# Performance work log

Hardware: AMD Instinct MI355X
Metric: run time of the kernel (lower is better)

## Reference

```python
import jax, jax.numpy as jnp
import numpy as np

N = 50000       # nodes
E = 600000      # directed edges (before self loops)
IN_CH = 128
HID = 64
HEADS = 2
H2_CH = HID // HEADS  # 32
OUT_CH = 96
NEG_SLOPE = 0.2


def _w(key, shape):
    fan_in = shape[-1]
    return jax.random.normal(key, shape, dtype=jnp.float32) / np.sqrt(fan_in).astype(np.float32)


def setup_inputs() -> dict:
    key = jax.random.key(0)
    ks = jax.random.split(key, 20)
    x = jax.random.normal(ks[0], (N, IN_CH), dtype=jnp.float32)
    edge_index = jax.random.randint(ks[1], (2, E), 0, N, dtype=jnp.int32)
    batch = jnp.zeros((N,), dtype=jnp.int32)
    return {
        "x": x, "edge_index": edge_index, "batch": batch,
        # lin_in 128->128
        "Win": _w(ks[2], (IN_CH, IN_CH)), "b_in": jnp.zeros((IN_CH,), jnp.float32),
        # conv1: GATv2Conv(128 -> 64, heads=2, concat=True)
        "Wl1": _w(ks[3], (HEADS * HID, IN_CH)), "bl1": jnp.zeros((HEADS * HID,), jnp.float32),
        "Wr1": _w(ks[4], (HEADS * HID, IN_CH)), "br1": jnp.zeros((HEADS * HID,), jnp.float32),
        "att1": _w(ks[5], (HEADS, HID)), "bias1": jnp.zeros((HEADS * HID,), jnp.float32),
        # conv2: GATv2Conv(128 -> 32, heads=1, concat=True)
        "Wl2": _w(ks[6], (H2_CH, HEADS * HID)), "bl2": jnp.zeros((H2_CH,), jnp.float32),
        "Wr2": _w(ks[7], (H2_CH, HEADS * HID)), "br2": jnp.zeros((H2_CH,), jnp.float32),
        "att2": _w(ks[8], (1, H2_CH)), "bias2": jnp.zeros((H2_CH,), jnp.float32),
        # final linear 32 -> 96
        "Wout": _w(ks[9], (OUT_CH, H2_CH)), "b_out": jnp.zeros((OUT_CH,), jnp.float32),
    }


def _segment_softmax(logits, seg, num):
    # logits: [E, H] grouped by seg (destination node); every node has a self loop.
    m = jax.ops.segment_max(logits, seg, num_segments=num)
    ex = jnp.exp(logits - m[seg])
    s = jax.ops.segment_sum(ex, seg, num_segments=num)
    return ex / s[seg]


def _gatv2_conv(h, Wl, bl, Wr, br, att, bias, src, dst, heads, ch):
    n = h.shape[0]
    xl = (h @ Wl.T + bl).reshape(n, heads, ch)  # source-side (x_j)
    xr = (h @ Wr.T + br).reshape(n, heads, ch)  # target-side (x_i)
    e = jax.nn.leaky_relu(xl[src] + xr[dst], NEG_SLOPE)       # [E, H, C]
    logits = jnp.einsum('ehc,hc->eh', e, att)                  # [E, H]
    alpha = _segment_softmax(logits, dst, n)                   # softmax over in-edges per dst
    out = jax.ops.segment_sum(alpha[:, :, None] * xl[src], dst, num_segments=n)
    return out.reshape(n, heads * ch) + bias


def reference(x, edge_index, batch, Win, b_in, Wl1, bl1, Wr1, br1, att1, bias1,
              Wl2, bl2, Wr2, br2, att2, bias2, Wout, b_out):
    n = x.shape[0]
    loops = jnp.arange(n, dtype=edge_index.dtype)
    src = jnp.concatenate([edge_index[0], loops])  # add_self_loops=True (PyG default)
    dst = jnp.concatenate([edge_index[1], loops])
    h = x @ Win.T + b_in
    h = jax.nn.relu(_gatv2_conv(h, Wl1, bl1, Wr1, br1, att1, bias1, src, dst, HEADS, HID))
    h = jax.nn.relu(_gatv2_conv(h, Wl2, bl2, Wr2, br2, att2, bias2, src, dst, 1, H2_CH))
    num_graphs = 1
    sums = jax.ops.segment_sum(h, batch, num_segments=num_graphs)          # [G, 32]
    cnt = jax.ops.segment_sum(jnp.ones((n,), h.dtype), batch, num_segments=num_graphs)
    pooled = sums / cnt[:, None]
    return pooled @ Wout.T + b_out  # [G, 96]
```

## Files before the change

### kernel.cpp

```cpp
#include <hip/hip_runtime.h>
#include <hip/hip_bf16.h>
#include <math.h>


#define NEG_SLOPE 0.2f
#define LOG2E 1.4426950408889634f
#define NREP 16
#define ELLW 64
#define CH 2048
#define CAPB 8192

typedef __attribute__((ext_vector_type(8))) short bf16x8;
typedef __attribute__((ext_vector_type(4))) float f32x4;

__device__ __forceinline__ float leaky(float t) { return fmaxf(t, NEG_SLOPE * t); }
__device__ __forceinline__ float bf2f(unsigned short u) {
    return __uint_as_float((unsigned)u << 16);
}
__device__ __forceinline__ short f2bf(float f) {
    __hip_bfloat16 h = __float2bfloat16(f);
    return *reinterpret_cast<short*>(&h);
}
__device__ __forceinline__ short f2bf_fast(float f) {
    return (short)((__float_as_uint(f) + 0x8000u) >> 16);
}

template <int CTRL>
__device__ __forceinline__ float dppadd(float v) {
    int t = __builtin_amdgcn_update_dpp(0, __float_as_int(v), CTRL, 0xF, 0xF, true);
    return v + __int_as_float(t);
}

__global__ __launch_bounds__(256) void prep_kernel(const float* __restrict__ Win,
                                                   const float* __restrict__ b_in,
                                                   const float* __restrict__ Wl1,
                                                   const float* __restrict__ bl1,
                                                   const float* __restrict__ Wr1,
                                                   const float* __restrict__ br1,
                                                   const float* __restrict__ Wl2,
                                                   const float* __restrict__ bl2,
                                                   const float* __restrict__ Wr2,
                                                   const float* __restrict__ br2,
                                                   unsigned short* __restrict__ Wcat1,
                                                   float* __restrict__ bcat1,
                                                   unsigned short* __restrict__ Wcat2,
                                                   float* __restrict__ bcat2,
                                                   int* __restrict__ bucketCnt,
                                                   float* __restrict__ pooledR, int N) {
    int b = blockIdx.x, t = threadIdx.x;
    if (b < 128) {
        int half = t >> 7;
        int k = t & 127;
        int o = b * 2 + half;
        const float* Wx = (o < 128) ? Wl1 : Wr1;
        const float* bx = (o < 128) ? bl1 : br1;
        int oo = o & 127;
        float acc = 0.f;
#pragma unroll 16
        for (int j = 0; j < 128; ++j)
            acc = fmaf(Wx[oo * 128 + j], Win[j * 128 + k], acc);
        Wcat1[o * 128 + k] = (unsigned short)f2bf(acc);

        __shared__ float red[256];
        red[t] = Wx[oo * 128 + k] * b_in[k];
        __syncthreads();
        for (int off = 64; off > 0; off >>= 1) {
            if (k < off) red[t] += red[t + off];
            __syncthreads();
        }
        if (k == 0) bcat1[o] = red[half * 128] + bx[oo];
    } else if (b < 160) {
        int i = (b - 128) * 256 + t;
        int m = i >> 7, kk = i & 127;
        float v = (m < 32) ? Wl2[m * 128 + kk] : Wr2[(m - 32) * 128 + kk];
        Wcat2[i] = (unsigned short)f2bf(v);
        if (b == 128 && t < 64) bcat2[t] = (t < 32) ? bl2[t] : br2[t - 32];
    } else if (b == 160) {
        if (t < 256) bucketCnt[t] = 0;
    } else {
        int i = (b - 161) * 256 + t;
        if (i < NREP * 32) pooledR[i] = 0.f;
    }
}

__global__ __launch_bounds__(256) void part_kernel(const int* __restrict__ ei,
                                                   int* __restrict__ bucketCnt,
                                                   unsigned int* __restrict__ region,
                                                   int E) {
    __shared__ int hist[256];
    __shared__ int base[256];
    __shared__ int off[256];
    int b = blockIdx.x, t = threadIdx.x;
    int e0 = b * CH;
    int e1 = e0 + CH; if (e1 > E) e1 = E;

    hist[t] = 0;
    __syncthreads();
    for (int e = e0 + t; e < e1; e += 256) {
        int d = ei[E + e];
        atomicAdd(&hist[d >> 8], 1);
    }
    __syncthreads();
    int h = hist[t];
    base[t] = (h > 0) ? atomicAdd(&bucketCnt[t], h) : 0;
    off[t] = 0;
    __syncthreads();
    for (int e = e0 + t; e < e1; e += 256) {
        int s = ei[e];
        int d = ei[E + e];
        int bk = d >> 8;
        int p = base[bk] + atomicAdd(&off[bk], 1);
        if (p < CAPB)
            region[(size_t)bk * CAPB + p] = (unsigned)s | ((unsigned)(d & 255) << 16);
    }
}

__global__ __launch_bounds__(256) void ellb_kernel(const unsigned int* __restrict__ region,
                                                   const int* __restrict__ bucketCnt,
                                                   unsigned short* __restrict__ ell,
                                                   int* __restrict__ deg, int N) {
    __shared__ unsigned short tile[256 * ELLW];
    __shared__ int cur[256];
    int nb = blockIdx.x, t = threadIdx.x;
    cur[t] = 0;
    __syncthreads();
    int cnt = bucketCnt[nb];
    if (cnt > CAPB) cnt = CAPB;
    for (int i = t; i < cnt; i += 256) {
        unsigned p = region[(size_t)nb * CAPB + i];
        int doff = p >> 16;
        int s = p & 0xFFFF;
        int r = atomicAdd(&cur[doff], 1);
        if (r < ELLW) tile[doff * ELLW + r] = (unsigned short)s;
    }
    __syncthreads();
    int node = nb * 256 + t;
    int dgl = cur[t];
    if (dgl > ELLW) dgl = ELLW;
    if (node < N) {
        deg[node] = dgl;
        int pe = dgl + 8; if (pe > ELLW) pe = ELLW;
        for (int r = dgl; r < pe; ++r) tile[t * ELLW + r] = (unsigned short)node;
    }
    __syncthreads();
    const uint4* tl = (const uint4*)tile;
    uint4* gl = (uint4*)(ell + (size_t)nb * 256 * ELLW);
#pragma unroll
    for (int k = 0; k < 8; ++k) {
        int idx = t + k * 256;
        int row = idx >> 3;
        if (nb * 256 + row < N) gl[idx] = tl[idx];
    }
}

__global__ __launch_bounds__(256) void gemm1_kernel(const float* __restrict__ x,
                                                    const unsigned short* __restrict__ W,
                                                    const float* __restrict__ bias,
                                                    unsigned short* __restrict__ XL,
                                                    unsigned short* __restrict__ XR, int N) {
    const int w = threadIdx.x >> 6;
    const int lane = threadIdx.x & 63;
    const int ln = lane & 15;
    const int quad = lane >> 4;
    const int nb = blockIdx.x * 32;
    const int c0 = w * 64;

    int rows[2];
#pragma unroll
    for (int rt = 0; rt < 2; ++rt) {
        int n = nb + rt * 16 + ln;
        rows[rt] = n < N ? n : N - 1;
    }

    float4 araw[2][4][2];
#pragma unroll
    for (int rt = 0; rt < 2; ++rt)
#pragma unroll
        for (int kc = 0; kc < 4; ++kc) {
            const float* p = x + (size_t)rows[rt] * 128 + kc * 32 + quad * 8;
            araw[rt][kc][0] = *(const float4*)p;
            araw[rt][kc][1] = *(const float4*)(p + 4);
        }
    bf16x8 a[2][4];
#pragma unroll
    for (int rt = 0; rt < 2; ++rt)
#pragma unroll
        for (int kc = 0; kc < 4; ++kc) {
            float4 u = araw[rt][kc][0], v = araw[rt][kc][1];
            a[rt][kc][0] = f2bf_fast(u.x); a[rt][kc][1] = f2bf_fast(u.y);
            a[rt][kc][2] = f2bf_fast(u.z); a[rt][kc][3] = f2bf_fast(u.w);
            a[rt][kc][4] = f2bf_fast(v.x); a[rt][kc][5] = f2bf_fast(v.y);
            a[rt][kc][6] = f2bf_fast(v.z); a[rt][kc][7] = f2bf_fast(v.w);
        }

    f32x4 acc[2][4];
#pragma unroll
    for (int rt = 0; rt < 2; ++rt)
#pragma unroll
        for (int ct = 0; ct < 4; ++ct) acc[rt][ct] = (f32x4){0.f, 0.f, 0.f, 0.f};

#pragma unroll
    for (int kc = 0; kc < 4; ++kc) {
        const int k0 = kc * 32 + quad * 8;
        bf16x8 wv[4];
#pragma unroll
        for (int ct = 0; ct < 4; ++ct)
            wv[ct] = *(const bf16x8*)(W + (size_t)(c0 + ct * 16 + ln) * 128 + k0);
#pragma unroll
        for (int rt = 0; rt < 2; ++rt)
#pragma unroll
            for (int ct = 0; ct < 4; ++ct)
                acc[rt][ct] = __builtin_amdgcn_mfma_f32_16x16x32_bf16(wv[ct], a[rt][kc], acc[rt][ct], 0, 0, 0);
    }

#pragma unroll
    for (int rt = 0; rt < 2; ++rt) {
        int n = nb + rt * 16 + ln;
        if (n >= N) continue;
#pragma unroll
        for (int ct = 0; ct < 4; ++ct) {
            int cb = c0 + ct * 16 + quad * 4;
            float4 bv = *(const float4*)&bias[cb];
            ushort4 o;
            o.x = (unsigned short)f2bf(acc[rt][ct][0] + bv.x);
            o.y = (unsigned short)f2bf(acc[rt][ct][1] + bv.y);
            o.z = (unsigned short)f2bf(acc[rt][ct][2] + bv.z);
            o.w = (unsigned short)f2bf(acc[rt][ct][3] + bv.w);
            if (cb < 128) *(ushort4*)&XL[(size_t)n * 128 + cb] = o;
            else          *(ushort4*)&XR[(size_t)n * 128 + cb - 128] = o;
        }
    }
}

__global__ __launch_bounds__(256) void node_conv1(const unsigned short* __restrict__ XL,
                                                  const unsigned short* __restrict__ XR,
                                                  const int* __restrict__ deg,
                                                  const unsigned short* __restrict__ ell,
                                                  const float* __restrict__ att,
                                                  const float* __restrict__ bias,
                                                  const unsigned short* __restrict__ Wcat2,
                                                  const float* __restrict__ bcat2,
                                                  unsigned short* __restrict__ XL2,
                                                  unsigned short* __restrict__ XR2, int N) {
    __shared__ unsigned short hsh[8 * 128];
    int g = threadIdx.x >> 5;
    int d = blockIdx.x * 8 + g;
    int l = threadIdx.x & 31;
    int c0 = 4 * l;

    if (d < N) {
        const unsigned short* row = ell + (size_t)d * ELLW;
        int re = deg[d];

        float4 attv = *(const float4*)&att[c0];
        attv.x *= LOG2E; attv.y *= LOG2E; attv.z *= LOG2E; attv.w *= LOG2E;
        ushort4 xru = *(const ushort4*)&XR[(size_t)d * 128 + c0];
        float xr0 = bf2f(xru.x), xr1 = bf2f(xru.y), xr2 = bf2f(xru.z), xr3 = bf2f(xru.w);

        float ssum, a0, a1, a2, a3;
        float w_self, xs0, xs1, xs2, xs3;

#define LOADX1(s) (*(const ushort4*)&XL[(size_t)(s) * 128 + c0])
#define PROC1(xu)                                                          \
    {                                                                      \
        float x0 = bf2f(xu.x), x1 = bf2f(xu.y), x2 = bf2f(xu.z), x3 = bf2f(xu.w); \
        float p = leaky(x0 + xr0) * attv.x;                                \
        p = fmaf(leaky(x1 + xr1), attv.y, p);                              \
        p = fmaf(leaky(x2 + xr2), attv.z, p);                              \
        p = fmaf(leaky(x3 + xr3), attv.w, p);                              \
        p = dppadd<0xB1>(p);                                               \
        p = dppadd<0x4E>(p);                                               \
        p = dppadd<0x124>(p);                                              \
        p = dppadd<0x128>(p);                                              \
        float wgt = exp2f(p);                                              \
        ssum += wgt;                                                       \
        a0 = fmaf(wgt, x0, a0); a1 = fmaf(wgt, x1, a1);                    \
        a2 = fmaf(wgt, x2, a2); a3 = fmaf(wgt, x3, a3);                    \
    }

        {
            ushort4 xu = *(const ushort4*)&XL[(size_t)d * 128 + c0];
            xs0 = bf2f(xu.x); xs1 = bf2f(xu.y); xs2 = bf2f(xu.z); xs3 = bf2f(xu.w);
            float p = leaky(xs0 + xr0) * attv.x;
            p = fmaf(leaky(xs1 + xr1), attv.y, p);
            p = fmaf(leaky(xs2 + xr2), attv.z, p);
            p = fmaf(leaky(xs3 + xr3), attv.w, p);
            p = dppadd<0xB1>(p);
            p = dppadd<0x4E>(p);
            p = dppadd<0x124>(p);
            p = dppadd<0x128>(p);
            w_self = exp2f(p);
            ssum = w_self;
            a0 = w_self * xs0; a1 = w_self * xs1;
            a2 = w_self * xs2; a3 = w_self * xs3;
        }
        if (re > 0) {
            int rp = (re + 3) & ~3;
            ushort4 i0 = *(const ushort4*)&row[0];
            ushort4 b0 = LOADX1(i0.x), b1 = LOADX1(i0.y), b2 = LOADX1(i0.z), b3 = LOADX1(i0.w);
            for (int j = 0; j < rp; j += 4) {
                int j4 = j + 4 < ELLW - 3 ? j + 4 : ELLW - 4;
                ushort4 i1 = *(const ushort4*)&row[j4];
                ushort4 n0 = LOADX1(i1.x), n1 = LOADX1(i1.y), n2 = LOADX1(i1.z), n3 = LOADX1(i1.w);
                PROC1(b0);
                PROC1(b1);
                PROC1(b2);
                PROC1(b3);
                b0 = n0; b1 = n1; b2 = n2; b3 = n3;
            }
            float kw = (float)(rp - re) * w_self;
            ssum -= kw;
            a0 = fmaf(-kw, xs0, a0); a1 = fmaf(-kw, xs1, a1);
            a2 = fmaf(-kw, xs2, a2); a3 = fmaf(-kw, xs3, a3);
        }
#undef PROC1
#undef LOADX1

        float inv = 1.0f / ssum;
        float4 bv = *(const float4*)&bias[c0];
        float r0 = fmaf(a0, inv, bv.x), r1 = fmaf(a1, inv, bv.y);
        float r2 = fmaf(a2, inv, bv.z), r3 = fmaf(a3, inv, bv.w);
        ushort4 o;
        o.x = (unsigned short)f2bf(r0 > 0.f ? r0 : 0.f);
        o.y = (unsigned short)f2bf(r1 > 0.f ? r1 : 0.f);
        o.z = (unsigned short)f2bf(r2 > 0.f ? r2 : 0.f);
        o.w = (unsigned short)f2bf(r3 > 0.f ? r3 : 0.f);
        *(ushort4*)&hsh[g * 128 + c0] = o;
    } else {
        *(ushort4*)&hsh[g * 128 + c0] = make_ushort4(0, 0, 0, 0);
    }
    __syncthreads();

    {
        int w = threadIdx.x >> 6;
        int lane = threadIdx.x & 63;
        int ln = lane & 15;
        int quad = lane >> 4;
        f32x4 acc = (f32x4){0.f, 0.f, 0.f, 0.f};
#pragma unroll
        for (int kc = 0; kc < 4; ++kc) {
            int k0 = kc * 32 + quad * 8;
            bf16x8 a;
            if (ln < 8) a = *(const bf16x8*)&hsh[ln * 128 + k0];
            else        a = (bf16x8){0, 0, 0, 0, 0, 0, 0, 0};
            bf16x8 wv = *(const bf16x8*)(Wcat2 + (size_t)(w * 16 + ln) * 128 + k0);
            acc = __builtin_amdgcn_mfma_f32_16x16x32_bf16(wv, a, acc, 0, 0, 0);
        }
        int n = blockIdx.x * 8 + ln;
        if (ln < 8 && n < N) {
            int cb = w * 16 + quad * 4;
            float4 bv = *(const float4*)&bcat2[cb];
            ushort4 o;
            o.x = (unsigned short)f2bf(acc[0] + bv.x);
            o.y = (unsigned short)f2bf(acc[1] + bv.y);
            o.z = (unsigned short)f2bf(acc[2] + bv.z);
            o.w = (unsigned short)f2bf(acc[3] + bv.w);
            if (cb < 32) *(ushort4*)&XL2[(size_t)n * 32 + cb] = o;
            else         *(ushort4*)&XR2[(size_t)n * 32 + cb - 32] = o;
        }
    }
}

__global__ __launch_bounds__(256) void node_conv2(const unsigned short* __restrict__ XL,
                                                  const unsigned short* __restrict__ XR,
                                                  const int* __restrict__ deg,
                                                  const unsigned short* __restrict__ ell,
                                                  const float* __restrict__ att,
                                                  const float* __restrict__ bias,
                                                  float* __restrict__ pooledR, int N) {
    __shared__ float psh[32];
    if (threadIdx.x < 32) psh[threadIdx.x] = 0.0f;
    __syncthreads();

    int slot = threadIdx.x >> 3;
    int l = threadIdx.x & 7;
    int c0 = 4 * l;
    float4 attv = *(const float4*)&att[c0];
    attv.x *= LOG2E; attv.y *= LOG2E; attv.z *= LOG2E; attv.w *= LOG2E;
    float4 bv = *(const float4*)&bias[c0];
    float p0 = 0.f, p1 = 0.f, p2 = 0.f, p3 = 0.f;

#define LOADX2(s) (*(const ushort4*)&XL[(size_t)(s) * 32 + c0])
#define PROC2(xu)                                                          \
    {                                                                      \
        float x0 = bf2f(xu.x), x1 = bf2f(xu.y), x2 = bf2f(xu.z), x3 = bf2f(xu.w); \
        float p = leaky(x0 + xr0) * attv.x;                                \
        p = fmaf(leaky(x1 + xr1), attv.y, p);                              \
        p = fmaf(leaky(x2 + xr2), attv.z, p);                              \
        p = fmaf(leaky(x3 + xr3), attv.w, p);                              \
        p = dppadd<0xB1>(p);                                               \
        p = dppadd<0x4E>(p);                                               \
        p = dppadd<0x141>(p);                                              \
        float wgt = exp2f(p);                                              \
        ssum += wgt;                                                       \
        a0 = fmaf(wgt, x0, a0); a1 = fmaf(wgt, x1, a1);                    \
        a2 = fmaf(wgt, x2, a2); a3 = fmaf(wgt, x3, a3);                    \
    }

    for (int d = blockIdx.x * 32 + slot; d < N; d += gridDim.x * 32) {
        const unsigned short* row = ell + (size_t)d * ELLW;
        int re = deg[d];
        ushort4 xru = *(const ushort4*)&XR[(size_t)d * 32 + c0];
        float xr0 = bf2f(xru.x), xr1 = bf2f(xru.y), xr2 = bf2f(xru.z), xr3 = bf2f(xru.w);
        float ssum, a0, a1, a2, a3;
        float w_self, xs0, xs1, xs2, xs3;

        {
            ushort4 xu = *(const ushort4*)&XL[(size_t)d * 32 + c0];
            xs0 = bf2f(xu.x); xs1 = bf2f(xu.y); xs2 = bf2f(xu.z); xs3 = bf2f(xu.w);
            float p = leaky(xs0 + xr0) * attv.x;
            p = fmaf(leaky(xs1 + xr1), attv.y, p);
            p = fmaf(leaky(xs2 + xr2), attv.z, p);
            p = fmaf(leaky(xs3 + xr3), attv.w, p);
            p = dppadd<0xB1>(p);
            p = dppadd<0x4E>(p);
            p = dppadd<0x141>(p);
            w_self = exp2f(p);
            ssum = w_self;
            a0 = w_self * xs0; a1 = w_self * xs1;
            a2 = w_self * xs2; a3 = w_self * xs3;
        }
        if (re > 0) {
            int rp = (re + 3) & ~3;
            ushort4 i0 = *(const ushort4*)&row[0];
            ushort4 b0 = LOADX2(i0.x), b1 = LOADX2(i0.y), b2 = LOADX2(i0.z), b3 = LOADX2(i0.w);
            for (int j = 0; j < rp; j += 4) {
                int j4 = j + 4 < ELLW - 3 ? j + 4 : ELLW - 4;
                ushort4 i1 = *(const ushort4*)&row[j4];
                ushort4 n0 = LOADX2(i1.x), n1 = LOADX2(i1.y), n2 = LOADX2(i1.z), n3 = LOADX2(i1.w);
                PROC2(b0);
                PROC2(b1);
                PROC2(b2);
                PROC2(b3);
                b0 = n0; b1 = n1; b2 = n2; b3 = n3;
            }
            float kw = (float)(rp - re) * w_self;
            ssum -= kw;
            a0 = fmaf(-kw, xs0, a0); a1 = fmaf(-kw, xs1, a1);
            a2 = fmaf(-kw, xs2, a2); a3 = fmaf(-kw, xs3, a3);
        }

        float inv = 1.0f / ssum;
        float r0 = fmaf(a0, inv, bv.x), r1 = fmaf(a1, inv, bv.y);
        float r2 = fmaf(a2, inv, bv.z), r3 = fmaf(a3, inv, bv.w);
        p0 += r0 > 0.f ? r0 : 0.f;
        p1 += r1 > 0.f ? r1 : 0.f;
        p2 += r2 > 0.f ? r2 : 0.f;
        p3 += r3 > 0.f ? r3 : 0.f;
    }
#undef PROC2
#undef LOADX2
    atomicAdd(&psh[c0 + 0], p0);
    atomicAdd(&psh[c0 + 1], p1);
    atomicAdd(&psh[c0 + 2], p2);
    atomicAdd(&psh[c0 + 3], p3);
    __syncthreads();
    float* rep = pooledR + (blockIdx.x & (NREP - 1)) * 32;
    if (threadIdx.x < 32) atomicAdd(&rep[threadIdx.x], psh[threadIdx.x]);
}

__global__ void out_kernel(const float* __restrict__ pooledR, const float* __restrict__ Wout,
                           const float* __restrict__ b_out, float* __restrict__ out, int N) {
    __shared__ float psum[32];
    if (threadIdx.x < 32) {
        float tot = 0.f;
#pragma unroll
        for (int r = 0; r < NREP; ++r) tot += pooledR[r * 32 + threadIdx.x];
        psum[threadIdx.x] = tot;
    }
    __syncthreads();
    int m = threadIdx.x;
    if (m < 96) {
        float invN = 1.0f / (float)N;
        float s = b_out[m];
#pragma unroll
        for (int c = 0; c < 32; ++c) s += (psum[c] * invN) * Wout[m * 32 + c];
        out[m] = s;
    }
}

extern "C" void kernel_launch(void* const* d_in, const int* in_sizes, int n_in,
                              void* d_out, int out_size, void* d_ws, size_t ws_size,
                              hipStream_t stream) {
    const float* x     = (const float*)d_in[0];
    const int*   ei    = (const int*)d_in[1];
    const float* Win   = (const float*)d_in[3];
    const float* b_in  = (const float*)d_in[4];
    const float* Wl1   = (const float*)d_in[5];
    const float* bl1   = (const float*)d_in[6];
    const float* Wr1   = (const float*)d_in[7];
    const float* br1   = (const float*)d_in[8];
    const float* att1  = (const float*)d_in[9];
    const float* bias1 = (const float*)d_in[10];
    const float* Wl2   = (const float*)d_in[11];
    const float* bl2   = (const float*)d_in[12];
    const float* Wr2   = (const float*)d_in[13];
    const float* br2   = (const float*)d_in[14];
    const float* att2  = (const float*)d_in[15];
    const float* bias2 = (const float*)d_in[16];
    const float* Wout  = (const float*)d_in[17];
    const float* b_out = (const float*)d_in[18];
    float* out = (float*)d_out;

    int N = in_sizes[0] / 128;
    int E = in_sizes[1] / 2;
    int NB = (N + 255) >> 8;

    char* wsb = (char*)d_ws;
    size_t off = 0;
    auto alloc = [&](size_t bytes) { void* p = wsb + off; off += (bytes + 255) & ~(size_t)255; return p; };

    unsigned short* XL1   = (unsigned short*)alloc((size_t)N * 128 * 2);
    unsigned short* XR1   = (unsigned short*)alloc((size_t)N * 128 * 2);
    unsigned short* XL2   = (unsigned short*)alloc((size_t)N * 32 * 2);
    unsigned short* XR2   = (unsigned short*)alloc((size_t)N * 32 * 2);
    unsigned short* Wcat1 = (unsigned short*)alloc(256 * 128 * 2);
    unsigned short* Wcat2 = (unsigned short*)alloc(64 * 128 * 2);
    float* bcat1   = (float*)alloc(256 * 4);
    float* bcat2   = (float*)alloc(64 * 4);
    float* pooledR = (float*)alloc(NREP * 32 * 4);
    int* bucketCnt = (int*)alloc(256 * 4);
    int* deg       = (int*)alloc((size_t)N * 4);
    unsigned int* region = (unsigned int*)alloc((size_t)NB * CAPB * 4);
    unsigned short* ell  = (unsigned short*)alloc((size_t)N * ELLW * 2);

    prep_kernel<<<163, 256, 0, stream>>>(Win, b_in, Wl1, bl1, Wr1, br1,
                                         Wl2, bl2, Wr2, br2,
                                         Wcat1, bcat1, Wcat2, bcat2, bucketCnt, pooledR, N);
    part_kernel<<<(E + CH - 1) / CH, 256, 0, stream>>>(ei, bucketCnt, region, E);
    ellb_kernel<<<NB, 256, 0, stream>>>(region, bucketCnt, ell, deg, N);
    gemm1_kernel<<<(N + 31) / 32, 256, 0, stream>>>(x, Wcat1, bcat1, XL1, XR1, N);
    node_conv1<<<(N + 7) / 8, 256, 0, stream>>>(XL1, XR1, deg, ell, att1, bias1,
                                                Wcat2, bcat2, XL2, XR2, N);
    node_conv2<<<1024, 256, 0, stream>>>(XL2, XR2, deg, ell, att2, bias2, pooledR, N);
    out_kernel<<<1, 128, 0, stream>>>(pooledR, Wout, b_out, out, N);
}
```

Measured before the change: 213.1 us.

## Fuse gemm1 blocks into partition and ELL-build kernels for overlap

The input projection GEMM is split in half, and each half runs as extra blocks inside the edge-partition and ELL-build kernels. This removes one launch and lets the latency-bound graph-preprocessing blocks overlap with the compute-heavy GEMM blocks. The node_conv2 grid also grows from 1024 blocks to one block per 32 nodes. A side effect is that the GEMM blocks in the second fused kernel reserve the ELL tile's large shared-memory allocation, which may lower their occupancy.

```diff
diff --git a/kernel.cpp b/kernel.cpp
--- a/kernel.cpp
+++ b/kernel.cpp
@@ -83,86 +83,16 @@
     }
 }
 
-__global__ __launch_bounds__(256) void part_kernel(const int* __restrict__ ei,
-                                                   int* __restrict__ bucketCnt,
-                                                   unsigned int* __restrict__ region,
-                                                   int E) {
-    __shared__ int hist[256];
-    __shared__ int base[256];
-    __shared__ int off[256];
-    int b = blockIdx.x, t = threadIdx.x;
-    int e0 = b * CH;
-    int e1 = e0 + CH; if (e1 > E) e1 = E;
-
-    hist[t] = 0;
-    __syncthreads();
-    for (int e = e0 + t; e < e1; e += 256) {
-        int d = ei[E + e];
-        atomicAdd(&hist[d >> 8], 1);
-    }
-    __syncthreads();
-    int h = hist[t];
-    base[t] = (h > 0) ? atomicAdd(&bucketCnt[t], h) : 0;
-    off[t] = 0;
-    __syncthreads();
-    for (int e = e0 + t; e < e1; e += 256) {
-        int s = ei[e];
-        int d = ei[E + e];
-        int bk = d >> 8;
-        int p = base[bk] + atomicAdd(&off[bk], 1);
-        if (p < CAPB)
-            region[(size_t)bk * CAPB + p] = (unsigned)s | ((unsigned)(d & 255) << 16);
-    }
-}
-
-__global__ __launch_bounds__(256) void ellb_kernel(const unsigned int* __restrict__ region,
-                                                   const int* __restrict__ bucketCnt,
-                                                   unsigned short* __restrict__ ell,
-                                                   int* __restrict__ deg, int N) {
-    __shared__ unsigned short tile[256 * ELLW];
-    __shared__ int cur[256];
-    int nb = blockIdx.x, t = threadIdx.x;
-    cur[t] = 0;
-    __syncthreads();
-    int cnt = bucketCnt[nb];
-    if (cnt > CAPB) cnt = CAPB;
-    for (int i = t; i < cnt; i += 256) {
-        unsigned p = region[(size_t)nb * CAPB + i];
-        int doff = p >> 16;
-        int s = p & 0xFFFF;
-        int r = atomicAdd(&cur[doff], 1);
-        if (r < ELLW) tile[doff * ELLW + r] = (unsigned short)s;
-    }
-    __syncthreads();
-    int node = nb * 256 + t;
-    int dgl = cur[t];
-    if (dgl > ELLW) dgl = ELLW;
-    if (node < N) {
-        deg[node] = dgl;
-        int pe = dgl + 8; if (pe > ELLW) pe = ELLW;
-        for (int r = dgl; r < pe; ++r) tile[t * ELLW + r] = (unsigned short)node;
-    }
-    __syncthreads();
-    const uint4* tl = (const uint4*)tile;
-    uint4* gl = (uint4*)(ell + (size_t)nb * 256 * ELLW);
-#pragma unroll
-    for (int k = 0; k < 8; ++k) {
-        int idx = t + k * 256;
-        int row = idx >> 3;
-        if (nb * 256 + row < N) gl[idx] = tl[idx];
-    }
-}
-
-__global__ __launch_bounds__(256) void gemm1_kernel(const float* __restrict__ x,
-                                                    const unsigned short* __restrict__ W,
-                                                    const float* __restrict__ bias,
-                                                    unsigned short* __restrict__ XL,
-                                                    unsigned short* __restrict__ XR, int N) {
+__device__ __forceinline__ void gemm1_body(const float* __restrict__ x,
+                                           const unsigned short* __restrict__ W,
+                                           const float* __restrict__ bias,
+                                           unsigned short* __restrict__ XL,
+                                           unsigned short* __restrict__ XR,
+                                           int N, int nb) {
     const int w = threadIdx.x >> 6;
     const int lane = threadIdx.x & 63;
     const int ln = lane & 15;
     const int quad = lane >> 4;
-    const int nb = blockIdx.x * 32;
     const int c0 = w * 64;
 
     int rows[2];
@@ -229,6 +159,96 @@
             if (cb < 128) *(ushort4*)&XL[(size_t)n * 128 + cb] = o;
             else          *(ushort4*)&XR[(size_t)n * 128 + cb - 128] = o;
         }
+    }
+}
+
+__global__ __launch_bounds__(256) void fuse1_kernel(const int* __restrict__ ei,
+                                                    int* __restrict__ bucketCnt,
+                                                    unsigned int* __restrict__ region,
+                                                    int E,
+                                                    const float* __restrict__ x,
+                                                    const unsigned short* __restrict__ W,
+                                                    const float* __restrict__ bias,
+                                                    unsigned short* __restrict__ XL,
+                                                    unsigned short* __restrict__ XR,
+                                                    int N, int PB) {
+    __shared__ int hist[256];
+    __shared__ int base[256];
+    __shared__ int off[256];
+    if (blockIdx.x >= PB) {
+        gemm1_body(x, W, bias, XL, XR, N, (blockIdx.x - PB) * 32);
+        return;
+    }
+    int b = blockIdx.x, t = threadIdx.x;
+    int e0 = b * CH;
+    int e1 = e0 + CH; if (e1 > E) e1 = E;
+
+    hist[t] = 0;
+    __syncthreads();
+    for (int e = e0 + t; e < e1; e += 256) {
+        int d = ei[E + e];
+        atomicAdd(&hist[d >> 8], 1);
+    }
+    __syncthreads();
+    int h = hist[t];
+    base[t] = (h > 0) ? atomicAdd(&bucketCnt[t], h) : 0;
+    off[t] = 0;
+    __syncthreads();
+    for (int e = e0 + t; e < e1; e += 256) {
+        int s = ei[e];
+        int d = ei[E + e];
+        int bk = d >> 8;
+        int p = base[bk] + atomicAdd(&off[bk], 1);
+        if (p < CAPB)
+            region[(size_t)bk * CAPB + p] = (unsigned)s | ((unsigned)(d & 255) << 16);
+    }
+}
+
+__global__ __launch_bounds__(256) void fuse2_kernel(const unsigned int* __restrict__ region,
+                                                    const int* __restrict__ bucketCnt,
+                                                    unsigned short* __restrict__ ell,
+                                                    int* __restrict__ deg,
+                                                    const float* __restrict__ x,
+                                                    const unsigned short* __restrict__ W,
+                                                    const float* __restrict__ bias,
+                                                    unsigned short* __restrict__ XL,
+                                                    unsigned short* __restrict__ XR,
+                                                    int N, int NB, int nodeOff) {
+    __shared__ unsigned short tile[256 * ELLW];
+    __shared__ int cur[256];
+    if (blockIdx.x >= NB) {
+        gemm1_body(x, W, bias, XL, XR, N, nodeOff + (blockIdx.x - NB) * 32);
+        return;
+    }
+    int nb = blockIdx.x, t = threadIdx.x;
+    cur[t] = 0;
+    __syncthreads();
+    int cnt = bucketCnt[nb];
+    if (cnt > CAPB) cnt = CAPB;
+    for (int i = t; i < cnt; i += 256) {
+        unsigned p = region[(size_t)nb * CAPB + i];
+        int doff = p >> 16;
+        int s = p & 0xFFFF;
+        int r = atomicAdd(&cur[doff], 1);
+        if (r < ELLW) tile[doff * ELLW + r] = (unsigned short)s;
+    }
+    __syncthreads();
+    int node = nb * 256 + t;
+    int dgl = cur[t];
+    if (dgl > ELLW) dgl = ELLW;
+    if (node < N) {
+        deg[node] = dgl;
+        int pe = dgl + 8; if (pe > ELLW) pe = ELLW;
+        for (int r = dgl; r < pe; ++r) tile[t * ELLW + r] = (unsigned short)node;
+    }
+    __syncthreads();
+    const uint4* tl = (const uint4*)tile;
+    uint4* gl = (uint4*)(ell + (size_t)nb * 256 * ELLW);
+#pragma unroll
+    for (int k = 0; k < 8; ++k) {
+        int idx = t + k * 256;
+        int row = idx >> 3;
+        if (nb * 256 + row < N) gl[idx] = tl[idx];
     }
 }
 
@@ -524,14 +544,20 @@
     unsigned int* region = (unsigned int*)alloc((size_t)NB * CAPB * 4);
     unsigned short* ell  = (unsigned short*)alloc((size_t)N * ELLW * 2);
 
+    int PB  = (E + CH - 1) / CH;
+    int GT  = (N + 31) / 32;
+    int GB1 = GT / 2;
+    int GB2 = GT - GB1;
+
     prep_kernel<<<163, 256, 0, stream>>>(Win, b_in, Wl1, bl1, Wr1, br1,
                                          Wl2, bl2, Wr2, br2,
                                          Wcat1, bcat1, Wcat2, bcat2, bucketCnt, pooledR, N);
-    part_kernel<<<(E + CH - 1) / CH, 256, 0, stream>>>(ei, bucketCnt, region, E);
-    ellb_kernel<<<NB, 256, 0, stream>>>(region, bucketCnt, ell, deg, N);
-    gemm1_kernel<<<(N + 31) / 32, 256, 0, stream>>>(x, Wcat1, bcat1, XL1, XR1, N);
+    fuse1_kernel<<<PB + GB1, 256, 0, stream>>>(ei, bucketCnt, region, E,
+                                               x, Wcat1, bcat1, XL1, XR1, N, PB);
+    fuse2_kernel<<<NB + GB2, 256, 0, stream>>>(region, bucketCnt, ell, deg,
+                                               x, Wcat1, bcat1, XL1, XR1, N, NB, GB1 * 32);
     node_conv1<<<(N + 7) / 8, 256, 0, stream>>>(XL1, XR1, deg, ell, att1, bias1,
                                                 Wcat2, bcat2, XL2, XR2, N);
-    node_conv2<<<1024, 256, 0, stream>>>(XL2, XR2, deg, ell, att2, bias2, pooledR, N);
+    node_conv2<<<GT, 256, 0, stream>>>(XL2, XR2, deg, ell, att2, bias2, pooledR, N);
     out_kernel<<<1, 128, 0, stream>>>(pooledR, Wout, b_out, out, N);
 }
```

Result: no change. 210.1 us (-1.4%).
